# Kernel optimization log

Hardware: AMD Instinct MI355X
Metric: run time of the kernel (lower is better)

## Reference

```python
import jax, jax.numpy as jnp
import numpy as np

B, T, C, H = 2, 2048, 1024, 16
DH = C // H  # 64


def setup_inputs() -> dict:
    key = jax.random.key(0)
    ks = jax.random.split(key, 8)
    scale = 1.0 / np.sqrt(C)
    x = jax.random.normal(ks[0], (B, T, C), dtype=jnp.float32)
    mask = jax.random.randint(ks[1], (B, T), 0, 2, dtype=jnp.int32)
    Wq = jax.random.normal(ks[2], (C, C), dtype=jnp.float32) * scale
    bq = jnp.zeros((C,), dtype=jnp.float32)
    Wk = jax.random.normal(ks[3], (C, C), dtype=jnp.float32) * scale
    bk = jnp.zeros((C,), dtype=jnp.float32)
    Wv = jax.random.normal(ks[4], (C, C), dtype=jnp.float32) * scale
    bv = jnp.zeros((C,), dtype=jnp.float32)
    return {"x": x, "Wq": Wq, "bq": bq, "Wk": Wk, "bk": bk, "Wv": Wv, "bv": bv, "mask": mask}


def reference(x, Wq, bq, Wk, bk, Wv, bv, mask):
    # q/k/v projections: [B,T,C] -> [B,H,T,DH]
    def proj(W, b):
        return (x @ W + b).reshape(B, T, H, DH).transpose(0, 2, 1, 3)

    q = proj(Wq, bq)
    k = proj(Wk, bk)
    v = proj(Wv, bv)

    att = jnp.einsum("bhqd,bhkd->bhqk", q, k) * (1.0 / np.sqrt(DH))

    # outer-product padding mask: square_mask[b,q,k] = mask[b,q]*mask[b,k]
    m = mask.astype(jnp.float32)
    square_mask = m[:, :, None] * m[:, None, :]           # [B,T,T]
    sm = (square_mask != 0)[:, None, :, :]                 # [B,1,T,T]
    att = jnp.where(sm, att, -jnp.inf)

    # rows that are fully masked (query token padded) -> softmax gives NaN
    # in torch; torch then zeros the NaNs. Replicate with a safe softmax.
    row_valid = (mask != 0)[:, None, :, None]              # [B,1,T,1]
    att_safe = jnp.where(row_valid, att, 0.0)
    att = jax.nn.softmax(att_safe, axis=-1)
    att = jnp.where(row_valid, att, 0.0)
    # attn_pdrop = 0.0 -> dropout is identity

    y = jnp.einsum("bhqk,bhkd->bhqd", att, v)              # [B,H,T,DH]
    y = y.transpose(0, 2, 1, 3).reshape(B, T, C)
    return y
```

## Files before the change

### kernel.cpp

```cpp
#include <hip/hip_runtime.h>

#define B_ 2
#define T_ 2048
#define C_ 1024
#define H_ 16
#define DH_ 64

typedef __attribute__((ext_vector_type(8))) _Float16 half8;
typedef __attribute__((ext_vector_type(2))) __fp16 fp16x2;
typedef __attribute__((ext_vector_type(4))) float f32x4;

__device__ __forceinline__ unsigned short f2h(float f) {
    union { _Float16 h; unsigned short u; } cv; cv.h = (_Float16)f; return cv.u;
}
__device__ __forceinline__ unsigned pk2(float a, float b) {
    union { fp16x2 h; unsigned u; } cv;
    cv.h = __builtin_amdgcn_cvt_pkrtz(a, b);
    return cv.u;
}

__device__ __forceinline__ void gll16(const void* g, void* l) {
    __builtin_amdgcn_global_load_lds(
        (const __attribute__((address_space(1))) void*)g,
        (__attribute__((address_space(3))) void*)l, 16, 0, 0);
}

__device__ __forceinline__ size_t kidx(int bh, int key, int d) {
    return ((size_t)(bh * 128 + (key >> 4)) * 2 + (d >> 5)) * 512
         + (size_t)((((d >> 3) & 3) * 16 + (key & 15)) * 8 + (d & 7));
}
__device__ __forceinline__ size_t vidx(int bh, int key, int d) {
    return (((size_t)(bh * 32 + (key >> 6)) * 4 + (d >> 4)) * 2 + ((key >> 5) & 1)) * 512
         + (size_t)((((key >> 3) & 3) * 16 + (d & 15)) * 8 + (key & 7));
}

__global__ __launch_bounds__(256) void prep_x_kernel(
    const float* __restrict__ x, unsigned short* __restrict__ xf,
    const int* __restrict__ mask, unsigned short* __restrict__ mb)
{
    const size_t idx8 = ((size_t)blockIdx.x * 256 + threadIdx.x) * 8;
    float4 v0 = *(const float4*)(x + idx8);
    float4 v1 = *(const float4*)(x + idx8 + 4);
    float f[8] = {v0.x, v0.y, v0.z, v0.w, v1.x, v1.y, v1.z, v1.w};
    unsigned short h[8];
#pragma unroll
    for (int i = 0; i < 8; i++) h[i] = f2h(f[i]);
    *(uint4*)(xf + idx8) = *(const uint4*)h;

    if (blockIdx.x == 0) {
#pragma unroll
        for (int j = 0; j < 16; j++) {
            int i = threadIdx.x * 16 + j;
            mb[i] = (mask[i] != 0) ? (unsigned short)0x3C00 : (unsigned short)0;
        }
    }
}

__global__ __launch_bounds__(256) void prep_w_kernel(
    const float* __restrict__ Wq, const float* __restrict__ Wk,
    const float* __restrict__ Wv, unsigned short* __restrict__ wt)
{
    __shared__ float tile[32][33];
    const int z = blockIdx.z;
    const float* __restrict__ W = (z == 0) ? Wq : (z == 1) ? Wk : Wv;
    unsigned short* __restrict__ wtz = wt + (size_t)z * C_ * C_;
    const int n0 = blockIdx.x * 32;
    const int k0 = blockIdx.y * 32;
    const int tx = threadIdx.x;
    const int ty = threadIdx.y;
#pragma unroll
    for (int j = 0; j < 4; j++)
        tile[ty + j * 8][tx] = W[(size_t)(k0 + ty + j * 8) * C_ + n0 + tx];
    __syncthreads();
#pragma unroll
    for (int j = 0; j < 4; j++)
        wtz[(size_t)(n0 + ty + j * 8) * C_ + k0 + tx] = f2h(tile[tx][ty + j * 8]);
}

__global__ __launch_bounds__(256) void qkv_mfma_kernel(
    const unsigned short* __restrict__ xf, const unsigned short* __restrict__ wt,
    const float* __restrict__ bq, const float* __restrict__ bk,
    const float* __restrict__ bv, const int* __restrict__ maskp,
    unsigned short* __restrict__ qb, unsigned short* __restrict__ kfr,
    unsigned short* __restrict__ vfr)
{
    __shared__ unsigned short sX[128 * 64];
    __shared__ unsigned short sW[128 * 64];

    const int z = blockIdx.z;
    const float* __restrict__ bias = (z == 0) ? bq : (z == 1) ? bk : bv;
    const unsigned short* __restrict__ wtz = wt + (size_t)z * C_ * C_;

    const int tok0 = blockIdx.x * 128;
    const int col0 = blockIdx.y * 128;
    const int wv    = threadIdx.x >> 6;
    const int lane  = threadIdx.x & 63;
    const int l15   = lane & 15;
    const int quad  = lane >> 4;
    const int l7    = l15 & 7;
    const int wm    = wv >> 1;
    const int wn    = wv & 1;
    const int lrow8 = lane >> 3;
    const int gch   = (lane & 7) ^ lrow8;

    f32x4 acc[4][4];
#pragma unroll
    for (int i = 0; i < 4; i++)
#pragma unroll
        for (int j = 0; j < 4; j++) acc[i][j] = (f32x4){0.f, 0.f, 0.f, 0.f};

    int aoff[4][2], boff[4][2];
#pragma unroll
    for (int i = 0; i < 4; i++)
#pragma unroll
        for (int s = 0; s < 2; s++) {
            aoff[i][s] = (wm * 64 + i * 16 + l15) * 64 + (((s * 4 + quad) ^ l7) * 8);
            boff[i][s] = (wn * 64 + i * 16 + l15) * 64 + (((s * 4 + quad) ^ l7) * 8);
        }

    const unsigned short* Abuf = (z < 2) ? sX : sW;
    const unsigned short* Bbuf = (z < 2) ? sW : sX;

    for (int k0 = 0; k0 < C_; k0 += 64) {
        __syncthreads();
#pragma unroll
        for (int s = 0; s < 8; ++s) {
            int g    = (s << 2) + wv;
            int tsel = g >> 4;
            int r0   = (g & 15) << 3;
            const unsigned short* src = tsel ? wtz : xf;
            unsigned short*       dst = tsel ? sW  : sX;
            int rowg = tsel ? col0 : tok0;
            gll16(src + (size_t)(rowg + r0 + lrow8) * C_ + k0 + gch * 8,
                  dst + r0 * 64);
        }
        __syncthreads();

        half8 af[4][2], bf_[4][2];
#pragma unroll
        for (int i = 0; i < 4; i++)
#pragma unroll
            for (int s = 0; s < 2; s++) {
                af[i][s]  = *(const half8*)&Abuf[aoff[i][s]];
                bf_[i][s] = *(const half8*)&Bbuf[boff[i][s]];
            }
#pragma unroll
        for (int s = 0; s < 2; s++)
#pragma unroll
            for (int j = 0; j < 4; j++)
#pragma unroll
                for (int i = 0; i < 4; i++)
                    acc[i][j] = __builtin_amdgcn_mfma_f32_16x16x32_f16(
                        af[i][s], bf_[j][s], acc[i][j], 0, 0, 0);
    }

    if (z == 0) {
#pragma unroll
        for (int j = 0; j < 4; j++) {
            int col = col0 + wn * 64 + j * 16 + l15;
            int h = col >> 6, d = col & 63;
            float bs = bias[col];
#pragma unroll
            for (int i = 0; i < 4; i++) {
#pragma unroll
                for (int r = 0; r < 4; r++) {
                    int tok = tok0 + wm * 64 + i * 16 + quad * 4 + r;
                    int bidx = tok >> 11, t = tok & (T_ - 1);
                    qb[((size_t)(bidx * H_ + h) * T_ + t) * DH_ + d] =
                        f2h(acc[i][j][r] + bs);
                }
            }
        }
    } else if (z == 1) {
#pragma unroll
        for (int j = 0; j < 4; j++) {
            int col = col0 + wn * 64 + j * 16 + l15;
            int h = col >> 6, d = col & 63;
            float bs = bias[col];
#pragma unroll
            for (int i = 0; i < 4; i++) {
#pragma unroll
                for (int r = 0; r < 4; r++) {
                    int tok = tok0 + wm * 64 + i * 16 + quad * 4 + r;
                    int bidx = tok >> 11, t = tok & (T_ - 1);
                    kfr[kidx(bidx * H_ + h, t, d)] = f2h(acc[i][j][r] + bs);
                }
            }
        }
    } else {
        float mv4[4]; int bidx4[4], t4[4];
#pragma unroll
        for (int j = 0; j < 4; j++) {
            int tok = tok0 + wn * 64 + j * 16 + l15;
            bidx4[j] = tok >> 11; t4[j] = tok & (T_ - 1);
            mv4[j] = (maskp[bidx4[j] * T_ + t4[j]] != 0) ? 1.f : 0.f;
        }
#pragma unroll
        for (int i = 0; i < 4; i++) {
#pragma unroll
            for (int r = 0; r < 4; r++) {
                int col = col0 + wm * 64 + i * 16 + quad * 4 + r;
                int h = col >> 6, d = col & 63;
                float bs = bias[col];
#pragma unroll
                for (int j = 0; j < 4; j++) {
                    vfr[vidx(bidx4[j] * H_ + h, t4[j], d)] =
                        f2h((acc[i][j][r] + bs) * mv4[j]);
                }
            }
        }
    }
}

__global__ __launch_bounds__(256) void attn_mfma_kernel(
    const unsigned short* __restrict__ qb,
    const unsigned short* __restrict__ kfr,
    const unsigned short* __restrict__ vfr,
    const int* __restrict__ mask,
    const unsigned short* __restrict__ mb,
    float* __restrict__ out)
{
    __shared__ unsigned short Ps[4][2][16 * 64];

    const int bh   = blockIdx.x;
    const int b    = bh >> 4;
    const int h    = bh & 15;
    const int wv   = threadIdx.x >> 6;
    const int lane = threadIdx.x & 63;
    const int l15  = lane & 15;
    const int quad = lane >> 4;
    const int l7   = l15 & 7;
    const int q0w  = blockIdx.y * 128 + wv * 32;

    const unsigned short* mbb = mb + b * T_;
    const int* __restrict__ mrow = mask + b * T_;

    const unsigned short* kfp = kfr + (size_t)bh * 131072 + lane * 8;
    const unsigned short* vfp = vfr + (size_t)bh * 131072 + lane * 8;

    half8 qf[2][2];
#pragma unroll
    for (int qt = 0; qt < 2; ++qt)
#pragma unroll
        for (int c = 0; c < 2; ++c)
            qf[qt][c] = *(const half8*)(qb + ((size_t)bh * T_ + q0w + qt * 16 + l15) * DH_
                                        + c * 32 + quad * 8);

    f32x4 o[2][4];
#pragma unroll
    for (int qt = 0; qt < 2; ++qt)
#pragma unroll
        for (int n = 0; n < 4; ++n) o[qt][n] = (f32x4){0.f, 0.f, 0.f, 0.f};
    f32x4 lacc[2];
    lacc[0] = (f32x4){0.f, 0.f, 0.f, 0.f};
    lacc[1] = (f32x4){0.f, 0.f, 0.f, 0.f};

    for (int kt = 0; kt < 32; ++kt) {
        const int kbase = kt * 64;

        half8 kf[4][2], vf[4][2];
#pragma unroll
        for (int s = 0; s < 8; ++s)
            kf[s >> 1][s & 1] = *(const half8*)(kfp + s * 512);
#pragma unroll
        for (int s = 0; s < 8; ++s)
            vf[s >> 1][s & 1] = *(const half8*)(vfp + s * 512);
        kfp += 4096; vfp += 4096;

        half8 bmf[2];
#pragma unroll
        for (int kc = 0; kc < 2; ++kc) {
            half8 mv = *(const half8*)(mbb + kbase + kc * 32 + quad * 8);
            bmf[kc] = (l15 == 0) ? mv : (half8)0;
        }

#pragma unroll
        for (int qt = 0; qt < 2; ++qt) {
            unsigned short* Pq = &Ps[wv][qt][0];

#pragma unroll
            for (int ktile = 0; ktile < 4; ++ktile) {
                f32x4 st = (f32x4){0.f, 0.f, 0.f, 0.f};
                st = __builtin_amdgcn_mfma_f32_16x16x32_f16(kf[ktile][0], qf[qt][0], st, 0, 0, 0);
                st = __builtin_amdgcn_mfma_f32_16x16x32_f16(kf[ktile][1], qf[qt][1], st, 0, 0, 0);
                float p0 = __builtin_amdgcn_exp2f(fminf(st[0] * 0.18033688011112042f, 14.f));
                float p1 = __builtin_amdgcn_exp2f(fminf(st[1] * 0.18033688011112042f, 14.f));
                float p2 = __builtin_amdgcn_exp2f(fminf(st[2] * 0.18033688011112042f, 14.f));
                float p3 = __builtin_amdgcn_exp2f(fminf(st[3] * 0.18033688011112042f, 14.f));
                uint2 pk;
                pk.x = pk2(p0, p1);
                pk.y = pk2(p2, p3);
                *(uint2*)(Pq + l15 * 64 + (((ktile * 2 + (quad >> 1)) ^ l7) * 8)
                          + (quad & 1) * 4) = pk;
            }

            half8 pf[2];
#pragma unroll
            for (int kc = 0; kc < 2; ++kc)
                pf[kc] = *(const half8*)(Pq + l15 * 64 + (((kc * 4 + quad) ^ l7) * 8));

            lacc[qt] = __builtin_amdgcn_mfma_f32_16x16x32_f16(pf[0], bmf[0], lacc[qt], 0, 0, 0);
            lacc[qt] = __builtin_amdgcn_mfma_f32_16x16x32_f16(pf[1], bmf[1], lacc[qt], 0, 0, 0);

#pragma unroll
            for (int n = 0; n < 4; ++n) {
#pragma unroll
                for (int kc = 0; kc < 2; ++kc)
                    o[qt][n] = __builtin_amdgcn_mfma_f32_16x16x32_f16(
                        pf[kc], vf[n][kc], o[qt][n], 0, 0, 0);
            }
        }
    }

#pragma unroll
    for (int qt = 0; qt < 2; ++qt) {
#pragma unroll
        for (int r = 0; r < 4; ++r) {
            float lv = __shfl(lacc[qt][r], quad << 4, 64);
            int q = q0w + qt * 16 + quad * 4 + r;
            float iv = (mrow[q] != 0 && lv > 0.f) ? (1.0f / lv) : 0.f;
            float* orow = out + ((size_t)(b * T_ + q)) * C_ + h * DH_;
#pragma unroll
            for (int n = 0; n < 4; ++n)
                orow[n * 16 + l15] = o[qt][n][r] * iv;
        }
    }
}

extern "C" void kernel_launch(void* const* d_in, const int* in_sizes, int n_in,
                              void* d_out, int out_size, void* d_ws, size_t ws_size,
                              hipStream_t stream)
{
    (void)in_sizes; (void)n_in; (void)out_size; (void)ws_size;
    const float* x  = (const float*)d_in[0];
    const float* Wq = (const float*)d_in[1];
    const float* bq = (const float*)d_in[2];
    const float* Wk = (const float*)d_in[3];
    const float* bk = (const float*)d_in[4];
    const float* Wv = (const float*)d_in[5];
    const float* bv = (const float*)d_in[6];
    const int* mask = (const int*)d_in[7];
    float* out = (float*)d_out;

    const size_t NX = (size_t)B_ * T_ * C_;
    unsigned short* xf  = (unsigned short*)d_ws;
    unsigned short* wt  = xf + NX;
    unsigned short* qb  = wt + (size_t)3 * C_ * C_;
    unsigned short* kfr = qb + NX;
    unsigned short* vfr = kfr + NX;
    unsigned short* mb  = vfr + NX;

    prep_x_kernel<<<2048, 256, 0, stream>>>(x, xf, mask, mb);
    prep_w_kernel<<<dim3(32, 32, 3), dim3(32, 8), 0, stream>>>(Wq, Wk, Wv, wt);
    qkv_mfma_kernel<<<dim3(32, 8, 3), 256, 0, stream>>>(
        xf, wt, bq, bk, bv, mask, qb, kfr, vfr);
    attn_mfma_kernel<<<dim3(32, 16), 256, 0, stream>>>(qb, kfr, vfr, mask, mb, out);
}
```

Baseline: 189.5 us.

## Double-buffer K/V loads, widen attention tile to 64 queries per wave, fold scale into Q

The attention kernel now keeps 64 queries per wave instead of 32, so each K/V tile loaded from global memory is reused across twice as many query rows. K/V register fragments are double-buffered so the loads for the next tile are issued while the current one is being computed. The softmax scale is folded into the Q projection epilogue, which removes a multiply per score. The cost is higher register pressure (launch bounds now set to one block), half as many blocks (256), and Q is stored pre-scaled in fp16.

```diff
diff --git a/kernel.cpp b/kernel.cpp
--- a/kernel.cpp
+++ b/kernel.cpp
@@ -167,7 +167,7 @@
                     int tok = tok0 + wm * 64 + i * 16 + quad * 4 + r;
                     int bidx = tok >> 11, t = tok & (T_ - 1);
                     qb[((size_t)(bidx * H_ + h) * T_ + t) * DH_ + d] =
-                        f2h(acc[i][j][r] + bs);
+                        f2h((acc[i][j][r] + bs) * 0.18033688011112042f);
                 }
             }
         }
@@ -212,7 +212,68 @@
     }
 }
 
-__global__ __launch_bounds__(256) void attn_mfma_kernel(
+__device__ __forceinline__ void load_kv(
+    const unsigned short* kfp, const unsigned short* vfp,
+    half8 (&kf)[4][2], half8 (&vf)[4][2])
+{
+#pragma unroll
+    for (int s = 0; s < 8; ++s)
+        kf[s >> 1][s & 1] = *(const half8*)(kfp + s * 512);
+#pragma unroll
+    for (int s = 0; s < 8; ++s)
+        vf[s >> 1][s & 1] = *(const half8*)(vfp + s * 512);
+}
+
+__device__ __forceinline__ void attn_step(
+    const half8 (&kf)[4][2], const half8 (&vf)[4][2],
+    const half8 (&qf)[4][2], const unsigned short* mbb, int kbase,
+    f32x4 (&o)[4][4], f32x4 (&lacc)[4], unsigned short* Pq,
+    int l15, int quad, int l7)
+{
+    half8 bmf[2];
+#pragma unroll
+    for (int kc = 0; kc < 2; ++kc) {
+        half8 mv = *(const half8*)(mbb + kbase + kc * 32 + quad * 8);
+        bmf[kc] = (l15 == 0) ? mv : (half8)0;
+    }
+
+#pragma unroll
+    for (int qt = 0; qt < 4; ++qt) {
+#pragma unroll
+        for (int ktile = 0; ktile < 4; ++ktile) {
+            f32x4 st = (f32x4){0.f, 0.f, 0.f, 0.f};
+            st = __builtin_amdgcn_mfma_f32_16x16x32_f16(kf[ktile][0], qf[qt][0], st, 0, 0, 0);
+            st = __builtin_amdgcn_mfma_f32_16x16x32_f16(kf[ktile][1], qf[qt][1], st, 0, 0, 0);
+            float p0 = __builtin_amdgcn_exp2f(fminf(st[0], 14.f));
+            float p1 = __builtin_amdgcn_exp2f(fminf(st[1], 14.f));
+            float p2 = __builtin_amdgcn_exp2f(fminf(st[2], 14.f));
+            float p3 = __builtin_amdgcn_exp2f(fminf(st[3], 14.f));
+            uint2 pk;
+            pk.x = pk2(p0, p1);
+            pk.y = pk2(p2, p3);
+            *(uint2*)(Pq + l15 * 64 + (((ktile * 2 + (quad >> 1)) ^ l7) * 8)
+                      + (quad & 1) * 4) = pk;
+        }
+
+        half8 pf[2];
+#pragma unroll
+        for (int kc = 0; kc < 2; ++kc)
+            pf[kc] = *(const half8*)(Pq + l15 * 64 + (((kc * 4 + quad) ^ l7) * 8));
+
+        lacc[qt] = __builtin_amdgcn_mfma_f32_16x16x32_f16(pf[0], bmf[0], lacc[qt], 0, 0, 0);
+        lacc[qt] = __builtin_amdgcn_mfma_f32_16x16x32_f16(pf[1], bmf[1], lacc[qt], 0, 0, 0);
+
+#pragma unroll
+        for (int n = 0; n < 4; ++n) {
+#pragma unroll
+            for (int kc = 0; kc < 2; ++kc)
+                o[qt][n] = __builtin_amdgcn_mfma_f32_16x16x32_f16(
+                    pf[kc], vf[n][kc], o[qt][n], 0, 0, 0);
+        }
+    }
+}
+
+__global__ __launch_bounds__(256, 1) void attn_mfma_kernel(
     const unsigned short* __restrict__ qb,
     const unsigned short* __restrict__ kfr,
     const unsigned short* __restrict__ vfr,
@@ -220,7 +281,7 @@
     const unsigned short* __restrict__ mb,
     float* __restrict__ out)
 {
-    __shared__ unsigned short Ps[4][2][16 * 64];
+    __shared__ unsigned short Ps[4][16 * 64];
 
     const int bh   = blockIdx.x;
     const int b    = bh >> 4;
@@ -230,90 +291,46 @@
     const int l15  = lane & 15;
     const int quad = lane >> 4;
     const int l7   = l15 & 7;
-    const int q0w  = blockIdx.y * 128 + wv * 32;
+    const int q0w  = blockIdx.y * 256 + wv * 64;
 
     const unsigned short* mbb = mb + b * T_;
     const int* __restrict__ mrow = mask + b * T_;
+    unsigned short* Pq = &Ps[wv][0];
 
     const unsigned short* kfp = kfr + (size_t)bh * 131072 + lane * 8;
     const unsigned short* vfp = vfr + (size_t)bh * 131072 + lane * 8;
 
-    half8 qf[2][2];
-#pragma unroll
-    for (int qt = 0; qt < 2; ++qt)
+    half8 qf[4][2];
+#pragma unroll
+    for (int qt = 0; qt < 4; ++qt)
 #pragma unroll
         for (int c = 0; c < 2; ++c)
             qf[qt][c] = *(const half8*)(qb + ((size_t)bh * T_ + q0w + qt * 16 + l15) * DH_
                                         + c * 32 + quad * 8);
 
-    f32x4 o[2][4];
-#pragma unroll
-    for (int qt = 0; qt < 2; ++qt)
+    f32x4 o[4][4];
+#pragma unroll
+    for (int qt = 0; qt < 4; ++qt)
 #pragma unroll
         for (int n = 0; n < 4; ++n) o[qt][n] = (f32x4){0.f, 0.f, 0.f, 0.f};
-    f32x4 lacc[2];
-    lacc[0] = (f32x4){0.f, 0.f, 0.f, 0.f};
-    lacc[1] = (f32x4){0.f, 0.f, 0.f, 0.f};
-
-    for (int kt = 0; kt < 32; ++kt) {
-        const int kbase = kt * 64;
-
-        half8 kf[4][2], vf[4][2];
-#pragma unroll
-        for (int s = 0; s < 8; ++s)
-            kf[s >> 1][s & 1] = *(const half8*)(kfp + s * 512);
-#pragma unroll
-        for (int s = 0; s < 8; ++s)
-            vf[s >> 1][s & 1] = *(const half8*)(vfp + s * 512);
-        kfp += 4096; vfp += 4096;
-
-        half8 bmf[2];
-#pragma unroll
-        for (int kc = 0; kc < 2; ++kc) {
-            half8 mv = *(const half8*)(mbb + kbase + kc * 32 + quad * 8);
-            bmf[kc] = (l15 == 0) ? mv : (half8)0;
-        }
-
-#pragma unroll
-        for (int qt = 0; qt < 2; ++qt) {
-            unsigned short* Pq = &Ps[wv][qt][0];
-
-#pragma unroll
-            for (int ktile = 0; ktile < 4; ++ktile) {
-                f32x4 st = (f32x4){0.f, 0.f, 0.f, 0.f};
-                st = __builtin_amdgcn_mfma_f32_16x16x32_f16(kf[ktile][0], qf[qt][0], st, 0, 0, 0);
-                st = __builtin_amdgcn_mfma_f32_16x16x32_f16(kf[ktile][1], qf[qt][1], st, 0, 0, 0);
-                float p0 = __builtin_amdgcn_exp2f(fminf(st[0] * 0.18033688011112042f, 14.f));
-                float p1 = __builtin_amdgcn_exp2f(fminf(st[1] * 0.18033688011112042f, 14.f));
-                float p2 = __builtin_amdgcn_exp2f(fminf(st[2] * 0.18033688011112042f, 14.f));
-                float p3 = __builtin_amdgcn_exp2f(fminf(st[3] * 0.18033688011112042f, 14.f));
-                uint2 pk;
-                pk.x = pk2(p0, p1);
-                pk.y = pk2(p2, p3);
-                *(uint2*)(Pq + l15 * 64 + (((ktile * 2 + (quad >> 1)) ^ l7) * 8)
-                          + (quad & 1) * 4) = pk;
-            }
-
-            half8 pf[2];
-#pragma unroll
-            for (int kc = 0; kc < 2; ++kc)
-                pf[kc] = *(const half8*)(Pq + l15 * 64 + (((kc * 4 + quad) ^ l7) * 8));
-
-            lacc[qt] = __builtin_amdgcn_mfma_f32_16x16x32_f16(pf[0], bmf[0], lacc[qt], 0, 0, 0);
-            lacc[qt] = __builtin_amdgcn_mfma_f32_16x16x32_f16(pf[1], bmf[1], lacc[qt], 0, 0, 0);
-
-#pragma unroll
-            for (int n = 0; n < 4; ++n) {
-#pragma unroll
-                for (int kc = 0; kc < 2; ++kc)
-                    o[qt][n] = __builtin_amdgcn_mfma_f32_16x16x32_f16(
-                        pf[kc], vf[n][kc], o[qt][n], 0, 0, 0);
-            }
-        }
-    }
-
-#pragma unroll
-    for (int qt = 0; qt < 2; ++qt) {
+    f32x4 lacc[4];
+#pragma unroll
+    for (int qt = 0; qt < 4; ++qt) lacc[qt] = (f32x4){0.f, 0.f, 0.f, 0.f};
+
+    half8 kA[4][2], vA[4][2], kB[4][2], vB[4][2];
+    load_kv(kfp, vfp, kA, vA);
+
+    for (int kt = 0; kt < 32; kt += 2) {
+        load_kv(kfp + 4096, vfp + 4096, kB, vB);
+        attn_step(kA, vA, qf, mbb, kt * 64, o, lacc, Pq, l15, quad, l7);
+        if (kt < 30)
+            load_kv(kfp + 8192, vfp + 8192, kA, vA);
+        attn_step(kB, vB, qf, mbb, (kt + 1) * 64, o, lacc, Pq, l15, quad, l7);
+        kfp += 8192; vfp += 8192;
+    }
+
+#pragma unroll
+    for (int qt = 0; qt < 4; ++qt) {
 #pragma unroll
         for (int r = 0; r < 4; ++r) {
             float lv = __shfl(lacc[qt][r], quad << 4, 64);
@@ -354,5 +371,5 @@
     prep_w_kernel<<<dim3(32, 32, 3), dim3(32, 8), 0, stream>>>(Wq, Wk, Wv, wt);
     qkv_mfma_kernel<<<dim3(32, 8, 3), 256, 0, stream>>>(
         xf, wt, bq, bk, bv, mask, qb, kfr, vfr);
-    attn_mfma_kernel<<<dim3(32, 16), 256, 0, stream>>>(qb, kfr, vfr, mask, mb, out);
-}
+    attn_mfma_kernel<<<dim3(32, 8), 256, 0, stream>>>(qb, kfr, vfr, mask, mb, out);
+}
```

New measurement: 185.7 us. 1.02x faster.
